# Kernel optimization log

Measured on AMD Instinct MI355X. Metric: run time of the kernel, lower is better.

The kernel has to match this reference:

```python
import jax, jax.numpy as jnp
import numpy as np

PS = 8; STRIDE = 4; KNN = 8; POOL_RATIO = 0.5; NHEADS = 4
EPS_BN = 1e-5; EPS_LN = 1e-5


def _conv(x, w, b):
    y = jax.lax.conv_general_dilated(x, w, (1, 1), ((1, 1), (1, 1)),
                                     dimension_numbers=('NCHW', 'OIHW', 'NCHW'))
    return y + b[None, :, None, None]


def _bn_eval(x, g, b):
    # BatchNorm2d in eval mode with running_mean=0, running_var=1
    return x * (g / np.sqrt(1.0 + EPS_BN))[None, :, None, None] + b[None, :, None, None]


def _maxpool2(x):
    return jax.lax.reduce_window(x, -jnp.inf, jax.lax.max, (1, 1, 2, 2), (1, 1, 2, 2), 'VALID')


def _layernorm(x, g, b):
    m = jnp.mean(x, axis=-1, keepdims=True)
    v = jnp.var(x, axis=-1, keepdims=True)
    return (x - m) / jnp.sqrt(v + EPS_LN) * g + b


def _mha(x, in_w, in_b, out_w, out_b):
    # batched self-attention, x: (B,S,E); matches nn.MultiheadAttention eval
    B, S, E = x.shape
    hd = E // NHEADS
    qkv = x @ in_w.T + in_b                      # (B,S,3E)
    q, k, v = jnp.split(qkv, 3, axis=-1)
    def heads(t):
        return t.reshape(B, S, NHEADS, hd).transpose(0, 2, 1, 3)
    q, k, v = heads(q), heads(k), heads(v)
    att = jax.nn.softmax(jnp.einsum('bhqd,bhkd->bhqk', q, k) / np.sqrt(hd), axis=-1)
    o = jnp.einsum('bhqk,bhkd->bhqd', att, v).transpose(0, 2, 1, 3).reshape(B, S, E)
    return o @ out_w.T + out_b


def _extract_patches(feat):
    # F.unfold(feat, kernel=PS, stride=STRIDE) -> (B, N, C*PS*PS), flat order (c, ki, kj)
    B, C, H, W = feat.shape
    nph = (H - PS) // STRIDE + 1
    npw = (W - PS) // STRIDE + 1
    hi = STRIDE * jnp.arange(nph)[:, None] + jnp.arange(PS)   # (nph, PS)
    wi = STRIDE * jnp.arange(npw)[:, None] + jnp.arange(PS)   # (npw, PS)
    p = feat[:, :, hi]            # (B,C,nph,PS,W)
    p = p[:, :, :, :, wi]         # (B,C,nph,PS,npw,PS)
    p = p.transpose(0, 2, 4, 1, 3, 5).reshape(B, nph * npw, C * PS * PS)
    return p, nph, npw


def _adjacency(nph, npw):
    # positions form a deterministic grid, identical across the batch -> static adjacency
    ii, jj = np.meshgrid(np.arange(nph), np.arange(npw), indexing='ij')
    pos = np.stack([ii.ravel(), jj.ravel()], axis=1).astype(np.float32)  # (N,2)
    N = pos.shape[0]
    d = np.linalg.norm(pos[:, None, :] - pos[None, :, :], axis=-1)
    order = np.argsort(d, axis=1, kind='stable')          # ascending; col 0 is self
    tgt = order[:, 1:KNN + 1]                             # (N, KNN)
    src = np.repeat(np.arange(N), KNN)
    adj = np.zeros((N, N), dtype=np.float32)
    adj[src, tgt.ravel()] = 1.0
    adj2 = ((adj @ adj) > 0).astype(np.float32)
    np.fill_diagonal(adj2, 0.0)
    return jnp.asarray(adj), jnp.asarray(adj2)


def setup_inputs() -> dict:
    key = jax.random.key(0)
    ks = jax.random.split(key, 16)
    def lin(k, o, i):
        return jax.random.normal(k, (o, i), jnp.float32) / np.sqrt(float(i))
    B = 16
    inp = {}
    inp['x'] = jax.random.normal(ks[0], (B, 3, 256, 256), jnp.float32)
    inp['conv1_w'] = jax.random.normal(ks[1], (64, 3, 3, 3), jnp.float32) / np.sqrt(27.0)
    inp['conv1_b'] = jnp.zeros((64,), jnp.float32)
    inp['bn1_g'] = jnp.ones((64,), jnp.float32); inp['bn1_b'] = jnp.zeros((64,), jnp.float32)
    inp['conv2_w'] = jax.random.normal(ks[2], (64, 64, 3, 3), jnp.float32) / np.sqrt(576.0)
    inp['conv2_b'] = jnp.zeros((64,), jnp.float32)
    inp['bn2_g'] = jnp.ones((64,), jnp.float32); inp['bn2_b'] = jnp.zeros((64,), jnp.float32)
    inp['proj_w'] = lin(ks[3], 128, 4096); inp['proj_b'] = jnp.zeros((128,), jnp.float32)
    inp['w1_w'] = lin(ks[4], 128, 128); inp['w1_b'] = jnp.zeros((128,), jnp.float32)
    inp['w2_w'] = lin(ks[5], 128, 128); inp['w2_b'] = jnp.zeros((128,), jnp.float32)
    inp['gate_w'] = lin(ks[6], 128, 256); inp['gate_b'] = jnp.zeros((128,), jnp.float32)
    inp['score_w'] = lin(ks[7], 1, 128); inp['score_b'] = jnp.zeros((1,), jnp.float32)
    inp['in_proj_w'] = lin(ks[8], 384, 128); inp['in_proj_b'] = jnp.zeros((384,), jnp.float32)
    inp['out_proj_w'] = lin(ks[9], 128, 128); inp['out_proj_b'] = jnp.zeros((128,), jnp.float32)
    inp['ff1_w'] = lin(ks[10], 512, 128); inp['ff1_b'] = jnp.zeros((512,), jnp.float32)
    inp['ff2_w'] = lin(ks[11], 128, 512); inp['ff2_b'] = jnp.zeros((128,), jnp.float32)
    inp['ln1_g'] = jnp.ones((128,), jnp.float32); inp['ln1_b'] = jnp.zeros((128,), jnp.float32)
    inp['ln2_g'] = jnp.ones((128,), jnp.float32); inp['ln2_b'] = jnp.zeros((128,), jnp.float32)
    inp['cls1_w'] = lin(ks[12], 64, 128); inp['cls1_b'] = jnp.zeros((64,), jnp.float32)
    inp['cls2_w'] = lin(ks[13], 2, 64); inp['cls2_b'] = jnp.zeros((2,), jnp.float32)
    return inp


def reference(x, conv1_w, conv1_b, bn1_g, bn1_b, conv2_w, conv2_b, bn2_g, bn2_b,
              proj_w, proj_b, w1_w, w1_b, w2_w, w2_b, gate_w, gate_b,
              score_w, score_b, in_proj_w, in_proj_b, out_proj_w, out_proj_b,
              ff1_w, ff1_b, ff2_w, ff2_b, ln1_g, ln1_b, ln2_g, ln2_b,
              cls1_w, cls1_b, cls2_w, cls2_b):
    # backbone
    feat = _maxpool2(jax.nn.relu(_bn_eval(_conv(x, conv1_w, conv1_b), bn1_g, bn1_b)))
    feat = _maxpool2(jax.nn.relu(_bn_eval(_conv(feat, conv2_w, conv2_b), bn2_g, bn2_b)))
    # patch graph construction (edges identical for every sample)
    patches, nph, npw = _extract_patches(feat)           # (B, N, 4096)
    adj1, adj2 = _adjacency(nph, npw)                    # (N, N) binary, static
    nodes = patches @ proj_w.T + proj_b                  # (B, N, 128)
    # multi-scale aggregation: index_add over edges == adj @ x (binary adjacency)
    z1 = jnp.einsum('ij,bjd->bid', adj1, nodes) @ w1_w.T + w1_b
    z2 = jnp.einsum('ij,bjd->bid', adj2, nodes) @ w2_w.T + w2_b
    g = jax.nn.sigmoid(jnp.concatenate([z1, z2], axis=-1) @ gate_w.T + gate_b)
    z = g * z1 + (1.0 - g) * z2                          # (B, N, 128)
    # hierarchical top-k pooling
    scores = (z @ score_w.T + score_b)[..., 0]           # (B, N)
    N = scores.shape[1]
    k = max(1, int(POOL_RATIO * N))
    _, idx = jax.lax.top_k(scores, k)                    # (B, k)
    pooled = jnp.take_along_axis(z, idx[..., None], axis=1)  # (B, k, 128)
    # graph transformer layer (dropout inactive in eval)
    h = _layernorm(pooled + _mha(pooled, in_proj_w, in_proj_b, out_proj_w, out_proj_b), ln1_g, ln1_b)
    ff = jax.nn.relu(h @ ff1_w.T + ff1_b) @ ff2_w.T + ff2_b
    h = _layernorm(h + ff, ln2_g, ln2_b)
    rep = jnp.sum(h, axis=1)                             # (B, 128)
    logits = jax.nn.relu(rep @ cls1_w.T + cls1_b) @ cls2_w.T + cls2_b
    return logits
```

## Files before the change

kernel.cpp:

```cpp
#include <hip/hip_runtime.h>
#include <hip/hip_bf16.h>
#include <math.h>

typedef unsigned short u16;
typedef unsigned int   u32;
typedef unsigned long long u64;
typedef __attribute__((ext_vector_type(8))) short short8v;
typedef __attribute__((ext_vector_type(4))) float f32x4;

__device__ __forceinline__ float bf2f(u16 u) {
  union { u32 i; float f; } v; v.i = ((u32)u) << 16; return v.f;
}
__device__ __forceinline__ u16 f2bf(float f) {
  union { float f; u32 i; } v; v.f = f;
  u32 r = (v.i + 0x7FFFu + ((v.i >> 16) & 1u)) >> 16;
  return (u16)r;
}

__global__ __launch_bounds__(256, 2) void k_conv1m(
    const float* __restrict__ x,
    const u16* __restrict__ wh, const u16* __restrict__ wl,
    const float* __restrict__ cb, const float* __restrict__ g, const float* __restrict__ bb,
    u16* __restrict__ feat1, int b0)
{
  __shared__ __align__(16) u16 sInH[3*18*18], sInL[3*18*18];
  __shared__ __align__(16) u16 sAh[256*40], sAl[256*40];
  __shared__ __align__(16) u16 sBh[64*40],  sBl[64*40];
  __shared__ float sBias[64];
  const int tx = blockIdx.x, ty = blockIdx.y, bl = blockIdx.z;
  const int b = b0 + bl;
  const int y0 = ty*16, x0 = tx*16;
  const int tid = threadIdx.x;
  const int w = tid >> 6, l = tid & 63, lr = l & 15, lk = l >> 4;

  if (tid < 64) {
    float sc = g[tid] * rsqrtf(1.0f + 1e-5f);
    sBias[tid] = cb[tid] * sc + bb[tid];
  }
  {
    const int oc = tid >> 2, seg = tid & 3;
    const int ps = seg ^ (oc & 3);
    *reinterpret_cast<uint4*>(&sBh[oc*40 + ps*8]) =
        *reinterpret_cast<const uint4*>(wh + oc*32 + seg*8);
    *reinterpret_cast<uint4*>(&sBl[oc*40 + ps*8]) =
        *reinterpret_cast<const uint4*>(wl + oc*32 + seg*8);
  }
  for (int i = tid; i < 3*18*18; i += 256) {
    const int c = i / 324, r = (i / 18) % 18, q = i % 18;
    const int yy = y0 - 1 + r, xx = x0 - 1 + q;
    float v = 0.f;
    if (yy >= 0 && yy < 256 && xx >= 0 && xx < 256)
      v = x[(((size_t)b*3 + c)*256 + yy)*256 + xx];
    const u16 h = f2bf(v);
    sInH[i] = h;
    sInL[i] = f2bf(v - bf2f(h));
  }
  __syncthreads();
  {
    const int py = tid >> 4, px = tid & 15;
    u32 hw[16], lw[16];
    #pragma unroll
    for (int i = 0; i < 16; i++) { hw[i] = 0u; lw[i] = 0u; }
    #pragma unroll
    for (int c = 0; c < 3; c++)
      #pragma unroll
      for (int ky = 0; ky < 3; ky++)
        #pragma unroll
        for (int kx = 0; kx < 3; kx++) {
          const int k = c*9 + ky*3 + kx;
          const int src = (c*18 + py + ky)*18 + px + kx;
          hw[k >> 1] |= ((u32)sInH[src]) << ((k & 1)*16);
          lw[k >> 1] |= ((u32)sInL[src]) << ((k & 1)*16);
        }
    #pragma unroll
    for (int s = 0; s < 4; s++) {
      const int ps = s ^ (tid & 3);
      uint4 vh, vl;
      vh.x = hw[s*4+0]; vh.y = hw[s*4+1]; vh.z = hw[s*4+2]; vh.w = hw[s*4+3];
      vl.x = lw[s*4+0]; vl.y = lw[s*4+1]; vl.z = lw[s*4+2]; vl.w = lw[s*4+3];
      *reinterpret_cast<uint4*>(&sAh[tid*40 + ps*8]) = vh;
      *reinterpret_cast<uint4*>(&sAl[tid*40 + ps*8]) = vl;
    }
  }
  __syncthreads();
  f32x4 acc[4][4];
  #pragma unroll
  for (int j = 0; j < 4; j++)
    #pragma unroll
    for (int ct = 0; ct < 4; ct++)
      acc[j][ct] = (f32x4){0.f,0.f,0.f,0.f};
  const int lkA = lk ^ (lr & 3);
  #pragma unroll
  for (int j = 0; j < 4; j++) {
    const int mt = w*4 + j;
    const short8v ah = *reinterpret_cast<const short8v*>(&sAh[(mt*16 + lr)*40 + lkA*8]);
    const short8v al = *reinterpret_cast<const short8v*>(&sAl[(mt*16 + lr)*40 + lkA*8]);
    #pragma unroll
    for (int ct = 0; ct < 4; ct++) {
      const short8v bh = *reinterpret_cast<const short8v*>(&sBh[(ct*16 + lr)*40 + lkA*8]);
      const short8v bv = *reinterpret_cast<const short8v*>(&sBl[(ct*16 + lr)*40 + lkA*8]);
      acc[j][ct] = __builtin_amdgcn_mfma_f32_16x16x32_bf16(ah, bh, acc[j][ct], 0, 0, 0);
      acc[j][ct] = __builtin_amdgcn_mfma_f32_16x16x32_bf16(ah, bv, acc[j][ct], 0, 0, 0);
      acc[j][ct] = __builtin_amdgcn_mfma_f32_16x16x32_bf16(al, bh, acc[j][ct], 0, 0, 0);
    }
  }
  #pragma unroll
  for (int j = 0; j < 2; j++) {
    const int jA = 2*j, jB = 2*j + 1;
    const int oy = ty*8 + w*2 + j;
    #pragma unroll
    for (int xh = 0; xh < 2; xh++) {
      const int ox = tx*8 + lk*2 + xh;
      #pragma unroll
      for (int ct = 0; ct < 4; ct++) {
        const int oc = ct*16 + lr;
        float m = fmaxf(fmaxf(acc[jA][ct][2*xh], acc[jA][ct][2*xh+1]),
                        fmaxf(acc[jB][ct][2*xh], acc[jB][ct][2*xh+1]));
        m = fmaxf(m + sBias[oc], 0.f);
        feat1[(((size_t)bl*128 + oy)*128 + ox)*64 + oc] = f2bf(m);
      }
    }
  }
}

__global__ __launch_bounds__(256, 2) void k_conv2m(
    const u16* __restrict__ feat1,
    const u16* __restrict__ wh, const u16* __restrict__ wl,
    const float* __restrict__ cb, const float* __restrict__ g, const float* __restrict__ bb,
    u16* __restrict__ feat2)
{
  __shared__ __align__(16) u16 sA[18*34*40];
  __shared__ __align__(16) u16 sBh[2][64*40], sBl[2][64*40];
  __shared__ float sBias[64];
  const int tx = blockIdx.x, ty = blockIdx.y, bl = blockIdx.z;
  const int y0 = ty*16, x0 = tx*32;
  const int tid = threadIdx.x;
  const int w = tid >> 6, l = tid & 63;
  const int lr = l & 15, lk = l >> 4;

  if (tid < 64) {
    float sc = g[tid] * rsqrtf(1.0f + 1e-5f);
    sBias[tid] = cb[tid] * sc + bb[tid];
  }

  f32x4 acc[8][4];
  #pragma unroll
  for (int j = 0; j < 8; j++)
    #pragma unroll
    for (int ct = 0; ct < 4; ct++)
      acc[j][ct] = (f32x4){0.f,0.f,0.f,0.f};

  const int ocB = tid >> 2;
  const int psB = (tid & 3) ^ (ocB & 3);
  uint4 rBh, rBl;
  auto ldB = [&](int chunk, int kk) {
    const size_t src = (size_t)(kk*2 + chunk)*2048 + tid*8;
    rBh = *reinterpret_cast<const uint4*>(wh + src);
    rBl = *reinterpret_cast<const uint4*>(wl + src);
  };
  auto stB = [&](int buf) {
    *reinterpret_cast<uint4*>(&sBh[buf][ocB*40 + psB*8]) = rBh;
    *reinterpret_cast<uint4*>(&sBl[buf][ocB*40 + psB*8]) = rBl;
  };

  const int lkB = lk ^ (lr & 3);
  for (int chunk = 0; chunk < 2; chunk++) {
    __syncthreads();
    ldB(chunk, 0);
    for (int idx = tid; idx < 612*4; idx += 256) {
      const int pix = idx >> 2, seg = idx & 3;
      const int r = pix / 34, cc = pix % 34;
      const int yy = y0 - 1 + r, xx = x0 - 1 + cc;
      uint4 v = {0u,0u,0u,0u};
      if (yy >= 0 && yy < 128 && xx >= 0 && xx < 128)
        v = *reinterpret_cast<const uint4*>(
              feat1 + (((size_t)bl*128 + yy)*128 + xx)*64 + chunk*32 + seg*8);
      const int ps = seg ^ (pix & 3);
      *reinterpret_cast<uint4*>(&sA[(size_t)pix*40 + ps*8]) = v;
    }
    stB(0);
    __syncthreads();
    int cur = 0;
    for (int kk = 0; kk < 9; kk++) {
      if (kk + 1 < 9) ldB(chunk, kk + 1);
      const int ky = kk / 3, kx = kk % 3;
      short8v a[8];
      #pragma unroll
      for (int j = 0; j < 8; j++) {
        const int m = w*8 + j;
        const int r = (m >> 1) + ky;
        const int cc = (m & 1)*16 + lr + kx;
        const int pixR = r*34 + cc;
        const int lkR = lk ^ (pixR & 3);
        a[j] = *reinterpret_cast<const short8v*>(&sA[(size_t)pixR*40 + lkR*8]);
      }
      #pragma unroll
      for (int ct = 0; ct < 4; ct++) {
        const short8v bh = *reinterpret_cast<const short8v*>(&sBh[cur][(ct*16 + lr)*40 + lkB*8]);
        const short8v bv = *reinterpret_cast<const short8v*>(&sBl[cur][(ct*16 + lr)*40 + lkB*8]);
        #pragma unroll
        for (int j = 0; j < 8; j++) {
          acc[j][ct] = __builtin_amdgcn_mfma_f32_16x16x32_bf16(a[j], bh, acc[j][ct], 0, 0, 0);
          acc[j][ct] = __builtin_amdgcn_mfma_f32_16x16x32_bf16(a[j], bv, acc[j][ct], 0, 0, 0);
        }
      }
      if (kk + 1 < 9) {
        stB(cur ^ 1);
        __syncthreads();
        cur ^= 1;
      }
    }
  }
  #pragma unroll
  for (int u = 0; u < 2; u++) {
    #pragma unroll
    for (int xh = 0; xh < 2; xh++) {
      const int jA = 4*u + xh, jB = 4*u + 2 + xh;
      #pragma unroll
      for (int ct = 0; ct < 4; ct++) {
        const int oc = ct*16 + lr;
        const float bias = sBias[oc];
        const float v0 = fmaxf(fmaxf(acc[jA][ct][0], acc[jA][ct][1]),
                               fmaxf(acc[jB][ct][0], acc[jB][ct][1]));
        const float v1 = fmaxf(fmaxf(acc[jA][ct][2], acc[jA][ct][3]),
                               fmaxf(acc[jB][ct][2], acc[jB][ct][3]));
        const u16 b0v = f2bf(fmaxf(v0 + bias, 0.f));
        const u16 b1v = f2bf(fmaxf(v1 + bias, 0.f));
        const int py = ty*8 + 2*w + u;
        const int px = tx*16 + xh*8 + lk*2;
        u32 pk = (u32)b0v | ((u32)b1v << 16);
        *reinterpret_cast<u32*>(&feat2[(((size_t)bl*64 + oc)*64 + py)*64 + px]) = pk;
      }
    }
  }
}

__global__ __launch_bounds__(256) void k_adj2(
    const int* __restrict__ nbr1, u64* __restrict__ mask2)
{
  const int i = threadIdx.x;
  if (i >= 225) return;
  u64 m0=0, m1=0, m2=0, m3=0;
  #pragma unroll
  for (int t = 0; t < 8; t++) {
    const int tt = nbr1[i*8 + t];
    #pragma unroll
    for (int u = 0; u < 8; u++) {
      const int j = nbr1[tt*8 + u];
      const u64 bset = 1ull << (j & 63);
      const int wd = j >> 6;
      m0 |= (wd == 0) ? bset : 0ull;
      m1 |= (wd == 1) ? bset : 0ull;
      m2 |= (wd == 2) ? bset : 0ull;
      m3 |= (wd == 3) ? bset : 0ull;
    }
  }
  {
    const u64 bc = ~(1ull << (i & 63));
    const int wd = i >> 6;
    if (wd == 0) m0 &= bc; else if (wd == 1) m1 &= bc;
    else if (wd == 2) m2 &= bc; else m3 &= bc;
  }
  mask2[i*4+0] = m0; mask2[i*4+1] = m1; mask2[i*4+2] = m2; mask2[i*4+3] = m3;
}

__global__ __launch_bounds__(256) void k_prep(
    const float* __restrict__ pjw, u16* __restrict__ pwh, u16* __restrict__ pwl,
    const float* __restrict__ c2w, const float* __restrict__ bn2g,
    u16* __restrict__ wc2h, u16* __restrict__ wc2l,
    const float* __restrict__ c1w, const float* __restrict__ bn1g,
    u16* __restrict__ wc1h, u16* __restrict__ wc1l,
    const float* __restrict__ ipw, float* __restrict__ iwt,
    const float* __restrict__ opw, float* __restrict__ owt,
    const float* __restrict__ f1w, float* __restrict__ f1wt,
    const float* __restrict__ f2w, float* __restrict__ f2wt,
    const float* __restrict__ w1w, float* __restrict__ w1t,
    const float* __restrict__ w2w, float* __restrict__ w2t,
    const float* __restrict__ gw,  float* __restrict__ gwt,
    int* __restrict__ nbr1)
{
  __shared__ int skey[256];
  __shared__ int sred[256];
  const int blk = blockIdx.x, tid = threadIdx.x;
  if (blk < 512) {
    const int i = (blk*256 + tid) * 4;
    float4 v = *reinterpret_cast<const float4*>(pjw + i);
    float e[4] = {v.x, v.y, v.z, v.w};
    ushort4 h, l;
    u16* hp = &h.x; u16* lp = &l.x;
    #pragma unroll
    for (int j = 0; j < 4; j++) {
      u16 hb = f2bf(e[j]);
      hp[j] = hb;
      lp[j] = f2bf(e[j] - bf2f(hb));
    }
    *reinterpret_cast<ushort4*>(pwh + i) = h;
    *reinterpret_cast<ushort4*>(pwl + i) = l;
  } else if (blk < 656) {
    const int d = (blk - 512)*256 + tid;
    if (d < 36864) {
      const int icL = d & 31, oc = (d >> 5) & 63, chunk = (d >> 11) & 1, kk = d >> 12;
      const float sc = bn2g[oc] * rsqrtf(1.0f + 1e-5f);
      const float val = c2w[((size_t)oc*64 + chunk*32 + icL)*9 + kk] * sc;
      const u16 hb = f2bf(val);
      wc2h[d] = hb;
      wc2l[d] = f2bf(val - bf2f(hb));
    }
  } else if (blk < 664) {
    const int d = (blk - 656)*256 + tid;
    if (d < 2048) {
      const int k = d & 31, oc = d >> 5;
      float val = 0.f;
      if (k < 27) val = c1w[oc*27 + k] * (bn1g[oc] * rsqrtf(1.0f + 1e-5f));
      const u16 hb = f2bf(val);
      wc1h[d] = hb;
      wc1l[d] = f2bf(val - bf2f(hb));
    }
  } else if (blk < 1688) {
    const float* src; float* dst; int O, K, base;
    if      (blk <  856) { src = ipw; dst = iwt;  O = 384; K = 128; base = 664;  }
    else if (blk <  920) { src = opw; dst = owt;  O = 128; K = 128; base = 856;  }
    else if (blk < 1176) { src = f1w; dst = f1wt; O = 512; K = 128; base = 920;  }
    else if (blk < 1432) { src = f2w; dst = f2wt; O = 128; K = 512; base = 1176; }
    else if (blk < 1496) { src = w1w; dst = w1t;  O = 128; K = 128; base = 1432; }
    else if (blk < 1560) { src = w2w; dst = w2t;  O = 128; K = 128; base = 1496; }
    else                 { src = gw;  dst = gwt;  O = 128; K = 256; base = 1560; }
    const int idx = (blk - base)*256 + tid;
    if (idx < O * K) {
      const int o = idx / K, k = idx % K;
      dst[(size_t)k * O + o] = src[idx];
    }
  } else {
    const int i = blk - 1688;
    int key = 0x7FFFFFFF;
    if (tid < 225 && tid != i) {
      const int di = i/15 - tid/15, dj = i%15 - tid%15;
      key = (di*di + dj*dj)*256 + tid;
    }
    skey[tid] = key;
    __syncthreads();
    for (int t = 0; t < 8; t++) {
      sred[tid] = skey[tid];
      __syncthreads();
      #pragma unroll
      for (int st = 128; st > 0; st >>= 1) {
        if (tid < st) sred[tid] = min(sred[tid], sred[tid+st]);
        __syncthreads();
      }
      const int wj = sred[0] & 255;
      if (tid == 0) nbr1[i*8 + t] = wj;
      __syncthreads();
      if (tid == wj) skey[tid] = 0x7FFFFFFF;
      __syncthreads();
    }
  }
}

__global__ __launch_bounds__(256, 2) void k_projm(
    const u16* __restrict__ feat2,
    const u16* __restrict__ pwh, const u16* __restrict__ pwl,
    float* __restrict__ partial, int b0)
{
  __shared__ __align__(16) u16 sBh[2][128*40];
  __shared__ __align__(16) u16 sBl[2][128*40];
  const int cx = blockIdx.x, kc = blockIdx.y, bl = blockIdx.z;
  const int b  = b0 + bl;
  const int n0 = cx * 64;
  const int rows = (225 - n0) < 64 ? (225 - n0) : 64;
  const int tid = threadIdx.x;
  const int w = tid >> 6, l = tid & 63;
  const int lr = l & 15, lk = l >> 4;

  f32x4 acc[8];
  #pragma unroll
  for (int i = 0; i < 8; i++) acc[i] = (f32x4){0.f, 0.f, 0.f, 0.f};

  int an = n0 + w*16 + lr;
  if (an > 224) an = 224;
  const int aph = an / 15, apw = an % 15;
  const int kbeg = kc * 512, kend = kbeg + 512;

  uint4 rBh[2], rBl[2];
  auto ldB = [&](int k0) {
    #pragma unroll
    for (int p = 0; p < 2; p++) {
      const int idx = p*256 + tid;
      const int col = idx >> 2, seg = idx & 3;
      const size_t off = (size_t)col*4096 + k0 + seg*8;
      rBh[p] = *reinterpret_cast<const uint4*>(pwh + off);
      rBl[p] = *reinterpret_cast<const uint4*>(pwl + off);
    }
  };
  auto stB = [&](int buf) {
    #pragma unroll
    for (int p = 0; p < 2; p++) {
      const int idx = p*256 + tid;
      const int col = idx >> 2, seg = idx & 3;
      const int ps = seg ^ (col & 3);
      *reinterpret_cast<uint4*>(&sBh[buf][col*40 + ps*8]) = rBh[p];
      *reinterpret_cast<uint4*>(&sBl[buf][col*40 + ps*8]) = rBl[p];
    }
  };

  const int lkB = lk ^ (lr & 3);
  ldB(kbeg);
  stB(0);
  __syncthreads();
  int cur = 0;
  for (int k0 = kbeg; k0 < kend; k0 += 32) {
    if (k0 + 32 < kend) ldB(k0 + 32);
    const int c = k0 >> 6;
    const int i = ((k0 & 32) >> 3) + lk;
    const u16* ap = feat2 + (((size_t)bl*64 + c)*64 + aph*4 + i)*64 + apw*4;
    union { short8v v; uint2 u[2]; } a;
    a.u[0] = *reinterpret_cast<const uint2*>(ap);
    a.u[1] = *reinterpret_cast<const uint2*>(ap + 4);
    #pragma unroll
    for (int ct = 0; ct < 8; ct++) {
      const short8v bh = *reinterpret_cast<const short8v*>(&sBh[cur][(ct*16 + lr)*40 + lkB*8]);
      const short8v bv = *reinterpret_cast<const short8v*>(&sBl[cur][(ct*16 + lr)*40 + lkB*8]);
      acc[ct] = __builtin_amdgcn_mfma_f32_16x16x32_bf16(a.v, bh, acc[ct], 0, 0, 0);
      acc[ct] = __builtin_amdgcn_mfma_f32_16x16x32_bf16(a.v, bv, acc[ct], 0, 0, 0);
    }
    if (k0 + 32 < kend) {
      stB(cur ^ 1);
      __syncthreads();
      cur ^= 1;
    }
  }
  #pragma unroll
  for (int ct = 0; ct < 8; ct++) {
    const int col = ct*16 + lr;
    #pragma unroll
    for (int v = 0; v < 4; v++) {
      const int r = w*16 + lk*4 + v;
      if (r < rows)
        partial[(((size_t)kc*16 + b)*225 + n0 + r)*128 + col] = acc[ct][v];
    }
  }
}

__global__ __launch_bounds__(128) void k_projr(
    const float* __restrict__ partial, const float* __restrict__ pb,
    float* __restrict__ nodes, int b0)
{
  const int n = blockIdx.x, bl = blockIdx.y;
  const int b = b0 + bl;
  const int d = threadIdx.x;
  float s = pb[d];
  #pragma unroll
  for (int kc = 0; kc < 8; kc++)
    s += partial[(((size_t)kc*16 + b)*225 + n)*128 + d];
  nodes[((size_t)b*225 + n)*128 + d] = s;
}

__global__ __launch_bounds__(256) void k_gz2(
    const float* __restrict__ nodes, const int* __restrict__ nbr1,
    const u64* __restrict__ mask2,
    const float* __restrict__ w1t, const float* __restrict__ w1b,
    const float* __restrict__ w2t, const float* __restrict__ w2b,
    const float* __restrict__ gwt, const float* __restrict__ gb,
    const float* __restrict__ sw, const float* __restrict__ sb,
    float* __restrict__ zbuf, float* __restrict__ scores)
{
  __shared__ float sA1[4][128], sA2[4][128], sC[4][256], sRed[4][128];
  const int row0 = blockIdx.x * 4;
  const int tid = threadIdx.x;
  const int d = tid & 127, rr = tid >> 7;
  #pragma unroll
  for (int q = 0; q < 2; q++) {
    const int lrow = rr*2 + q;
    const int row = row0 + lrow;
    const int b = row / 225, n = row % 225;
    const float* nb = nodes + (size_t)b * 225 * 128;
    float a1 = 0.f;
    #pragma unroll
    for (int t = 0; t < 8; t++) a1 += nb[(size_t)nbr1[n*8+t]*128 + d];
    float a2 = 0.f;
    for (int wd = 0; wd < 4; wd++) {
      u64 m = mask2[n*4 + wd];
      while (m) {
        int j = wd*64 + __builtin_ctzll(m);
        a2 += nb[(size_t)j*128 + d];
        m &= m - 1;
      }
    }
    sA1[lrow][d] = a1; sA2[lrow][d] = a2;
  }
  __syncthreads();
  float z1[2], z2[2];
  { const float b1 = w1b[d], b2 = w2b[d];
    z1[0] = b1; z1[1] = b1; z2[0] = b2; z2[1] = b2; }
  #pragma unroll 4
  for (int k = 0; k < 128; k++) {
    const float wv1 = w1t[k*128 + d];
    const float wv2 = w2t[k*128 + d];
    #pragma unroll
    for (int q = 0; q < 2; q++) {
      z1[q] += wv1 * sA1[rr*2 + q][k];
      z2[q] += wv2 * sA2[rr*2 + q][k];
    }
  }
  #pragma unroll
  for (int q = 0; q < 2; q++) {
    sC[rr*2 + q][d] = z1[q]; sC[rr*2 + q][128 + d] = z2[q];
  }
  __syncthreads();
  float gl[2];
  { const float bg = gb[d]; gl[0] = bg; gl[1] = bg; }
  #pragma unroll 4
  for (int k = 0; k < 256; k++) {
    const float wv = gwt[k*128 + d];
    #pragma unroll
    for (int q = 0; q < 2; q++)
      gl[q] += wv * sC[rr*2 + q][k];
  }
  const float swd = sw[d];
  #pragma unroll
  for (int q = 0; q < 2; q++) {
    const int row = row0 + rr*2 + q;
    const float gg = 1.f / (1.f + expf(-gl[q]));
    const float zv = gg * z1[q] + (1.f - gg) * z2[q];
    zbuf[(size_t)row*128 + d] = zv;
    sRed[rr*2 + q][d] = zv * swd;
  }
  __syncthreads();
  if (tid < 64) {
    const int r = tid >> 4, j = tid & 15;
    float part = 0.f;
    #pragma unroll
    for (int i = 0; i < 8; i++) part += sRed[r][j*8 + i];
    #pragma unroll
    for (int m = 8; m >= 1; m >>= 1) part += __shfl_xor(part, m, 64);
    if (j == 0) scores[row0 + r] = part + sb[0];
  }
}

__global__ __launch_bounds__(256) void k_topk(
    const float* __restrict__ scores, int* __restrict__ sel)
{
  __shared__ float ss[225];
  const int b = blockIdx.x, tid = threadIdx.x;
  if (tid < 112) sel[b*112 + tid] = tid;
  if (tid < 225) ss[tid] = scores[b*225 + tid];
  __syncthreads();
  if (tid < 225) {
    float s = ss[tid];
    int rank = 0;
    for (int j = 0; j < 225; j++) {
      float sj = ss[j];
      rank += (sj > s) || (sj == s && j < tid);
    }
    if (rank < 112) sel[b*112 + rank] = tid;
  }
}

__global__ __launch_bounds__(256) void k_qkv(
    const float* __restrict__ zbuf, const int* __restrict__ sel,
    const float* __restrict__ iwt, const float* __restrict__ ib,
    float* __restrict__ q, float* __restrict__ k, float* __restrict__ v)
{
  __shared__ float sx[7][128];
  const int s0 = blockIdx.x * 7, b = blockIdx.y;
  const int tid = threadIdx.x;
  const int c = tid & 127, half = tid >> 7;
  const int r0 = half * 4;
  const int nr = half ? 3 : 4;

  for (int idx = tid; idx < 7*128; idx += 256) {
    const int r = idx >> 7, dd = idx & 127;
    int row = sel[b*112 + s0 + r];
    row = row < 0 ? 0 : (row > 224 ? 224 : row);
    sx[r][dd] = zbuf[((size_t)b*225 + row)*128 + dd];
  }
  __syncthreads();

  float acc[3][4];
  #pragma unroll
  for (int p = 0; p < 3; p++)
    #pragma unroll
    for (int rr = 0; rr < 4; rr++) acc[p][rr] = ib[p*128 + c];
  for (int kk = 0; kk < 128; kk++) {
    float wv[3];
    #pragma unroll
    for (int p = 0; p < 3; p++) wv[p] = iwt[kk*384 + p*128 + c];
    #pragma unroll
    for (int rr = 0; rr < 4; rr++) {
      const int rowi = (r0 + rr < 7) ? (r0 + rr) : 6;
      const float xv = sx[rowi][kk];
      #pragma unroll
      for (int p = 0; p < 3; p++) acc[p][rr] += wv[p] * xv;
    }
  }
  const int h = c >> 5, t = c & 31;
  float* outs[3] = {q, k, v};
  #pragma unroll
  for (int p = 0; p < 3; p++)
    #pragma unroll
    for (int rr = 0; rr < 4; rr++)
      if (rr < nr)
        outs[p][(((size_t)b*4 + h)*112 + s0 + r0 + rr)*32 + t] = acc[p][rr];
}

__global__ __launch_bounds__(256) void k_attn(
    const float* __restrict__ q, const float* __restrict__ k,
    const float* __restrict__ v, float* __restrict__ o)
{
  __shared__ float sK[112*33], sV[112*33];
  __shared__ float sQ[14*33];
  __shared__ float sP[14][112];
  const int qc = blockIdx.x, h = blockIdx.y, b = blockIdx.z;
  const size_t base = ((size_t)b*4 + h) * 112 * 32;
  const int tid = threadIdx.x;
  for (int i = tid; i < 112*32; i += 256) {
    const int r = i >> 5, c = i & 31;
    sK[r*33 + c] = k[base + i];
    sV[r*33 + c] = v[base + i];
  }
  for (int i = tid; i < 14*32; i += 256) {
    const int r = i >> 5, c = i & 31;
    sQ[r*33 + c] = q[base + (size_t)(qc*14)*32 + i];
  }
  __syncthreads();
  const int qg = tid >> 4, j = tid & 15;
  if (qg < 14) {
    const float scale = 0.17677669529663687f;
    float pv[7];
    float mx = -INFINITY;
    #pragma unroll
    for (int t7 = 0; t7 < 7; t7++) {
      const int kk = j + t7*16;
      float s = 0.f;
      #pragma unroll
      for (int t = 0; t < 32; t++) s += sQ[qg*33 + t] * sK[kk*33 + t];
      pv[t7] = s * scale;
      mx = fmaxf(mx, pv[t7]);
    }
    #pragma unroll
    for (int m = 8; m >= 1; m >>= 1) mx = fmaxf(mx, __shfl_xor(mx, m, 16));
    float lsum = 0.f;
    #pragma unroll
    for (int t7 = 0; t7 < 7; t7++) { pv[t7] = expf(pv[t7] - mx); lsum += pv[t7]; }
    #pragma unroll
    for (int m = 8; m >= 1; m >>= 1) lsum += __shfl_xor(lsum, m, 16);
    const float inv = 1.f / lsum;
    #pragma unroll
    for (int t7 = 0; t7 < 7; t7++) sP[qg][j + t7*16] = pv[t7] * inv;
  }
  __syncthreads();
  if (qg < 14) {
    const int s = qc*14 + qg;
    float o0 = 0.f, o1 = 0.f;
    for (int kk = 0; kk < 112; kk++) {
      const float p = sP[qg][kk];
      o0 += p * sV[kk*33 + j];
      o1 += p * sV[kk*33 + j + 16];
    }
    float* op = o + ((size_t)b*112 + s)*128 + h*32;
    op[j] = o0;
    op[j + 16] = o1;
  }
}

__global__ __launch_bounds__(256) void k_tail(
    const float* __restrict__ o, const float* __restrict__ zbuf,
    const int* __restrict__ sel,
    const float* __restrict__ owt, const float* __restrict__ ob,
    const float* __restrict__ l1g, const float* __restrict__ l1b,
    const float* __restrict__ f1wt, const float* __restrict__ f1b,
    const float* __restrict__ f2wt, const float* __restrict__ f2b,
    const float* __restrict__ l2g, const float* __restrict__ l2b,
    float* __restrict__ h2)
{
  __shared__ float sO[7][128];
  __shared__ float sh[7][128];
  __shared__ float sf[7][512];
  __shared__ float sV[7][128];
  __shared__ float sMean[7], sRstd[7];
  const int s0 = blockIdx.x * 7, b = blockIdx.y;
  const int tid = threadIdx.x;
  const int d = tid & 127, half = tid >> 7;
  const int r0 = half * 4;
  const int nr = half ? 3 : 4;

  for (int idx = tid; idx < 7*128; idx += 256) {
    const int r = idx >> 7, dd = idx & 127;
    sO[r][dd] = o[((size_t)b*112 + s0 + r)*128 + dd];
  }
  __syncthreads();
  {
    float acc[4];
    #pragma unroll
    for (int rr = 0; rr < 4; rr++) acc[rr] = ob[d];
    for (int kk = 0; kk < 128; kk++) {
      const float wv = owt[kk*128 + d];
      #pragma unroll
      for (int rr = 0; rr < 4; rr++) {
        const int rowi = (r0 + rr < 7) ? (r0 + rr) : 6;
        acc[rr] += wv * sO[rowi][kk];
      }
    }
    #pragma unroll
    for (int rr = 0; rr < 4; rr++) {
      if (rr < nr) {
        int row = sel[b*112 + s0 + r0 + rr];
        row = row < 0 ? 0 : (row > 224 ? 224 : row);
        acc[rr] += zbuf[((size_t)b*225 + row)*128 + d];
        sV[r0 + rr][d] = acc[rr];
      }
    }
  }
  __syncthreads();
  {
    const int r = tid >> 4, j = tid & 15;
    if (r < 7) {
      float p1 = 0.f, p2 = 0.f;
      #pragma unroll
      for (int i = 0; i < 8; i++) { float v = sV[r][j*8 + i]; p1 += v; p2 += v*v; }
      #pragma unroll
      for (int m = 8; m >= 1; m >>= 1) {
        p1 += __shfl_xor(p1, m, 64);
        p2 += __shfl_xor(p2, m, 64);
      }
      if (j == 0) {
        const float mean = p1 * (1.f/128.f);
        sMean[r] = mean;
        sRstd[r] = rsqrtf(p2 * (1.f/128.f) - mean*mean + 1e-5f);
      }
    }
  }
  __syncthreads();
  for (int idx = tid; idx < 7*128; idx += 256) {
    const int r = idx >> 7, dd = idx & 127;
    sh[r][dd] = (sV[r][dd] - sMean[r]) * sRstd[r] * l1g[dd] + l1b[dd];
  }
  __syncthreads();

  {
    float a0[7], a1[7];
    const float b0 = f1b[tid], b1 = f1b[tid + 256];
    #pragma unroll
    for (int r = 0; r < 7; r++) { a0[r] = b0; a1[r] = b1; }
    for (int kk = 0; kk < 128; kk++) {
      const float w0 = f1wt[kk*512 + tid];
      const float w1 = f1wt[kk*512 + tid + 256];
      #pragma unroll
      for (int r = 0; r < 7; r++) {
        const float xv = sh[r][kk];
        a0[r] += w0 * xv;
        a1[r] += w1 * xv;
      }
    }
    #pragma unroll
    for (int r = 0; r < 7; r++) {
      sf[r][tid]       = fmaxf(a0[r], 0.f);
      sf[r][tid + 256] = fmaxf(a1[r], 0.f);
    }
  }
  __syncthreads();
  {
    float acc[4];
    #pragma unroll
    for (int rr = 0; rr < 4; rr++) acc[rr] = f2b[d];
    for (int kk = 0; kk < 512; kk++) {
      const float wv = f2wt[kk*128 + d];
      #pragma unroll
      for (int rr = 0; rr < 4; rr++) {
        const int rowi = (r0 + rr < 7) ? (r0 + rr) : 6;
        acc[rr] += wv * sf[rowi][kk];
      }
    }
    #pragma unroll
    for (int rr = 0; rr < 4; rr++)
      if (rr < nr)
        sV[r0 + rr][d] = sh[r0 + rr][d] + acc[rr];
  }
  __syncthreads();
  {
    const int r = tid >> 4, j = tid & 15;
    if (r < 7) {
      float p1 = 0.f, p2 = 0.f;
      #pragma unroll
      for (int i = 0; i < 8; i++) { float v = sV[r][j*8 + i]; p1 += v; p2 += v*v; }
      #pragma unroll
      for (int m = 8; m >= 1; m >>= 1) {
        p1 += __shfl_xor(p1, m, 64);
        p2 += __shfl_xor(p2, m, 64);
      }
      if (j == 0) {
        const float mean = p1 * (1.f/128.f);
        sMean[r] = mean;
        sRstd[r] = rsqrtf(p2 * (1.f/128.f) - mean*mean + 1e-5f);
      }
    }
  }
  __syncthreads();
  for (int idx = tid; idx < 7*128; idx += 256) {
    const int r = idx >> 7, dd = idx & 127;
    h2[((size_t)b*112 + s0 + r)*128 + dd] =
        (sV[r][dd] - sMean[r]) * sRstd[r] * l2g[dd] + l2b[dd];
  }
}

__global__ __launch_bounds__(64) void k_cls(
    const float* __restrict__ h2,
    const float* __restrict__ c1w, const float* __restrict__ c1b,
    const float* __restrict__ c2w, const float* __restrict__ c2b,
    float* __restrict__ out)
{
  __shared__ float sr[128], sc[64];
  const int b = blockIdx.x, tid = threadIdx.x;
  float r0 = 0.f, r1 = 0.f;
  for (int s2 = 0; s2 < 112; s2++) {
    const float* row = h2 + ((size_t)b*112 + s2)*128;
    r0 += row[tid];
    r1 += row[tid + 64];
  }
  sr[tid] = r0; sr[tid + 64] = r1;
  __syncthreads();
  float acc = c1b[tid];
  const float* wr = c1w + (size_t)tid * 128;
  for (int kk = 0; kk < 128; kk++) acc += wr[kk] * sr[kk];
  sc[tid] = fmaxf(acc, 0.f);
  __syncthreads();
  if (tid < 2) {
    float l = c2b[tid];
    for (int kk = 0; kk < 64; kk++) l += c2w[tid*64 + kk] * sc[kk];
    out[b*2 + tid] = l;
  }
}

extern "C" void kernel_launch(void* const* d_in, const int* in_sizes, int n_in,
                              void* d_out, int out_size, void* d_ws, size_t ws_size,
                              hipStream_t stream)
{
  const float* x    = (const float*)d_in[0];
  const float* c1w  = (const float*)d_in[1];
  const float* c1b  = (const float*)d_in[2];
  const float* bn1g = (const float*)d_in[3];
  const float* bn1b = (const float*)d_in[4];
  const float* c2w  = (const float*)d_in[5];
  const float* c2b  = (const float*)d_in[6];
  const float* bn2g = (const float*)d_in[7];
  const float* bn2b = (const float*)d_in[8];
  const float* pjw  = (const float*)d_in[9];
  const float* pjb  = (const float*)d_in[10];
  const float* w1w  = (const float*)d_in[11];
  const float* w1b  = (const float*)d_in[12];
  const float* w2w  = (const float*)d_in[13];
  const float* w2b  = (const float*)d_in[14];
  const float* gw   = (const float*)d_in[15];
  const float* gb   = (const float*)d_in[16];
  const float* scw  = (const float*)d_in[17];
  const float* scb  = (const float*)d_in[18];
  const float* ipw  = (const float*)d_in[19];
  const float* ipb  = (const float*)d_in[20];
  const float* opw  = (const float*)d_in[21];
  const float* opb  = (const float*)d_in[22];
  const float* f1w  = (const float*)d_in[23];
  const float* f1b  = (const float*)d_in[24];
  const float* f2w  = (const float*)d_in[25];
  const float* f2b  = (const float*)d_in[26];
  const float* l1g  = (const float*)d_in[27];
  const float* l1b  = (const float*)d_in[28];
  const float* l2g  = (const float*)d_in[29];
  const float* l2b  = (const float*)d_in[30];
  const float* cl1w = (const float*)d_in[31];
  const float* cl1b = (const float*)d_in[32];
  const float* cl2w = (const float*)d_in[33];
  const float* cl2b = (const float*)d_in[34];

  char* p = (char*)d_ws;
  auto alloc = [&](size_t n) { char* r = p; p += (n + 255) & ~(size_t)255; return r; };
  u64*   mask2  = (u64*)  alloc(900    * sizeof(u64));
  int*   nbr1   = (int*)  alloc(1800   * sizeof(int));
  int*   sel    = (int*)  alloc(1792   * sizeof(int));
  float* scores = (float*)alloc(3600   * sizeof(float));
  u16*   pwh    = (u16*)  alloc(524288 * sizeof(u16));
  u16*   pwl    = (u16*)  alloc(524288 * sizeof(u16));
  u16*   wc2h   = (u16*)  alloc(36864  * sizeof(u16));
  u16*   wc2l   = (u16*)  alloc(36864  * sizeof(u16));
  u16*   wc1h   = (u16*)  alloc(2048   * sizeof(u16));
  u16*   wc1l   = (u16*)  alloc(2048   * sizeof(u16));
  float* iwt    = (float*)alloc(49152  * sizeof(float));
  float* owt    = (float*)alloc(16384  * sizeof(float));
  float* f1wt   = (float*)alloc(65536  * sizeof(float));
  float* f2wt   = (float*)alloc(65536  * sizeof(float));
  float* w1t    = (float*)alloc(16384  * sizeof(float));
  float* w2t    = (float*)alloc(16384  * sizeof(float));
  float* gwt    = (float*)alloc(32768  * sizeof(float));
  float* partial= (float*)alloc(8ull*16*225*128 * sizeof(float));
  float* zbuf   = (float*)alloc(460800 * sizeof(float));
  float* nodes  = (float*)alloc(460800 * sizeof(float));
  const size_t fixed_bytes = (size_t)(p - (char*)d_ws);

  const size_t qkv_bytes = 3ull * 229376ull * sizeof(float);
  const size_t per_batch = 64ull*128*128*2 + 64ull*64*64*2;
  int BC = 16;
  size_t s3 = 0;
  for (;; BC >>= 1) {
    s3 = (size_t)BC * per_batch; if (s3 < qkv_bytes) s3 = qkv_bytes;
    if (fixed_bytes + s3 + 65536 <= ws_size) break;
    if (BC == 1) { return; }
  }
  char* S3 = alloc(s3);

  u16*   feat1 = (u16*)S3;
  u16*   feat2 = (u16*)(S3 + (size_t)BC * 2097152ull);
  float* qb    = (float*)S3;
  float* kb    = qb + 229376;
  float* vb    = kb + 229376;
  float* obuf  = nodes;
  float* hbuf  = nodes + 229376;

  k_prep<<<1913, 256, 0, stream>>>(pjw, pwh, pwl, c2w, bn2g, wc2h, wc2l,
                                   c1w, bn1g, wc1h, wc1l,
                                   ipw, iwt, opw, owt, f1w, f1wt, f2w, f2wt,
                                   w1w, w1t, w2w, w2t, gw, gwt, nbr1);
  k_adj2<<<1, 256, 0, stream>>>(nbr1, mask2);

  for (int b0 = 0; b0 < 16; b0 += BC) {
    k_conv1m<<<dim3(16,16,BC), 256, 0, stream>>>(x, wc1h, wc1l, c1b, bn1g, bn1b, feat1, b0);
    k_conv2m<<<dim3(4,8,BC), 256, 0, stream>>>(feat1, wc2h, wc2l, c2b, bn2g, bn2b, feat2);
    k_projm <<<dim3(4,8,BC), 256, 0, stream>>>(feat2, pwh, pwl, partial, b0);
    k_projr <<<dim3(225,BC), 128, 0, stream>>>(partial, pjb, nodes, b0);
  }

  k_gz2  <<<900, 256, 0, stream>>>(nodes, nbr1, mask2, w1t, w1b, w2t, w2b,
                                   gwt, gb, scw, scb, zbuf, scores);
  k_topk <<<16, 256, 0, stream>>>(scores, sel);
  k_qkv  <<<dim3(16,16), 256, 0, stream>>>(zbuf, sel, iwt, ipb, qb, kb, vb);
  k_attn <<<dim3(8,4,16), 256, 0, stream>>>(qb, kb, vb, obuf);
  k_tail <<<dim3(16,16), 256, 0, stream>>>(obuf, zbuf, sel, owt, opb, l1g, l1b,
                                           f1wt, f1b, f2wt, f2b, l2g, l2b, hbuf);
  k_cls  <<<16, 64, 0, stream>>>(hbuf, cl1w, cl1b, cl2w, cl2b, (float*)d_out);
}
```

Before: 260.6 us.

## Split projection GEMM tiles to 32 rows with 2x2 warp layout and prefetch A

The projection GEMM kernel now handles 32 node rows per block instead of 64, and its four waves are arranged as 2 row groups by 2 column groups, each owning 4 column tiles. The grid doubles along x, launch bounds allow 4 blocks per CU, and the A operand for the next k-step is loaded early alongside B. The goal is more blocks and higher occupancy for this small GEMM, plus hiding global A-load latency. In exchange, each B tile in shared memory is now loaded by twice as many blocks.

```diff
diff --git a/kernel.cpp b/kernel.cpp
--- a/kernel.cpp
+++ b/kernel.cpp
@@ -356,7 +356,7 @@
   }
 }
 
-__global__ __launch_bounds__(256, 2) void k_projm(
+__global__ __launch_bounds__(256, 4) void k_projm(
     const u16* __restrict__ feat2,
     const u16* __restrict__ pwh, const u16* __restrict__ pwl,
     float* __restrict__ partial, int b0)
@@ -365,17 +365,19 @@
   __shared__ __align__(16) u16 sBl[2][128*40];
   const int cx = blockIdx.x, kc = blockIdx.y, bl = blockIdx.z;
   const int b  = b0 + bl;
-  const int n0 = cx * 64;
-  const int rows = (225 - n0) < 64 ? (225 - n0) : 64;
+  const int n0 = cx * 32;
+  const int rows = (225 - n0) < 32 ? (225 - n0) : 32;
   const int tid = threadIdx.x;
   const int w = tid >> 6, l = tid & 63;
   const int lr = l & 15, lk = l >> 4;
-
-  f32x4 acc[8];
-  #pragma unroll
-  for (int i = 0; i < 8; i++) acc[i] = (f32x4){0.f, 0.f, 0.f, 0.f};
-
-  int an = n0 + w*16 + lr;
+  const int wr = w & 1;
+  const int wc = w >> 1;
+
+  f32x4 acc[4];
+  #pragma unroll
+  for (int i = 0; i < 4; i++) acc[i] = (f32x4){0.f, 0.f, 0.f, 0.f};
+
+  int an = n0 + wr*16 + lr;
   if (an > 224) an = 224;
   const int aph = an / 15, apw = an % 15;
   const int kbeg = kc * 512, kend = kbeg + 512;
@@ -401,41 +403,49 @@
       *reinterpret_cast<uint4*>(&sBl[buf][col*40 + ps*8]) = rBl[p];
     }
   };
-
-  const int lkB = lk ^ (lr & 3);
-  ldB(kbeg);
-  stB(0);
-  __syncthreads();
-  int cur = 0;
-  for (int k0 = kbeg; k0 < kend; k0 += 32) {
-    if (k0 + 32 < kend) ldB(k0 + 32);
+  auto ldA = [&](int k0, uint2& a0, uint2& a1) {
     const int c = k0 >> 6;
     const int i = ((k0 & 32) >> 3) + lk;
     const u16* ap = feat2 + (((size_t)bl*64 + c)*64 + aph*4 + i)*64 + apw*4;
+    a0 = *reinterpret_cast<const uint2*>(ap);
+    a1 = *reinterpret_cast<const uint2*>(ap + 4);
+  };
+
+  const int lkB = lk ^ (lr & 3);
+  uint2 a0c, a1c, a0n, a1n;
+  ldB(kbeg);
+  ldA(kbeg, a0c, a1c);
+  stB(0);
+  __syncthreads();
+  int cur = 0;
+  for (int k0 = kbeg; k0 < kend; k0 += 32) {
+    const bool more = (k0 + 32 < kend);
+    if (more) { ldB(k0 + 32); ldA(k0 + 32, a0n, a1n); }
     union { short8v v; uint2 u[2]; } a;
-    a.u[0] = *reinterpret_cast<const uint2*>(ap);
-    a.u[1] = *reinterpret_cast<const uint2*>(ap + 4);
-    #pragma unroll
-    for (int ct = 0; ct < 8; ct++) {
+    a.u[0] = a0c; a.u[1] = a1c;
+    #pragma unroll
+    for (int c4 = 0; c4 < 4; c4++) {
+      const int ct = wc*4 + c4;
       const short8v bh = *reinterpret_cast<const short8v*>(&sBh[cur][(ct*16 + lr)*40 + lkB*8]);
       const short8v bv = *reinterpret_cast<const short8v*>(&sBl[cur][(ct*16 + lr)*40 + lkB*8]);
-      acc[ct] = __builtin_amdgcn_mfma_f32_16x16x32_bf16(a.v, bh, acc[ct], 0, 0, 0);
-      acc[ct] = __builtin_amdgcn_mfma_f32_16x16x32_bf16(a.v, bv, acc[ct], 0, 0, 0);
-    }
-    if (k0 + 32 < kend) {
+      acc[c4] = __builtin_amdgcn_mfma_f32_16x16x32_bf16(a.v, bh, acc[c4], 0, 0, 0);
+      acc[c4] = __builtin_amdgcn_mfma_f32_16x16x32_bf16(a.v, bv, acc[c4], 0, 0, 0);
+    }
+    if (more) {
       stB(cur ^ 1);
       __syncthreads();
       cur ^= 1;
-    }
-  }
-  #pragma unroll
-  for (int ct = 0; ct < 8; ct++) {
-    const int col = ct*16 + lr;
+      a0c = a0n; a1c = a1n;
+    }
+  }
+  #pragma unroll
+  for (int c4 = 0; c4 < 4; c4++) {
+    const int col = (wc*4 + c4)*16 + lr;
     #pragma unroll
     for (int v = 0; v < 4; v++) {
-      const int r = w*16 + lk*4 + v;
+      const int r = wr*16 + lk*4 + v;
       if (r < rows)
-        partial[(((size_t)kc*16 + b)*225 + n0 + r)*128 + col] = acc[ct][v];
+        partial[(((size_t)kc*16 + b)*225 + n0 + r)*128 + col] = acc[c4][v];
     }
   }
 }
@@ -922,7 +932,7 @@
   for (int b0 = 0; b0 < 16; b0 += BC) {
     k_conv1m<<<dim3(16,16,BC), 256, 0, stream>>>(x, wc1h, wc1l, c1b, bn1g, bn1b, feat1, b0);
     k_conv2m<<<dim3(4,8,BC), 256, 0, stream>>>(feat1, wc2h, wc2l, c2b, bn2g, bn2b, feat2);
-    k_projm <<<dim3(4,8,BC), 256, 0, stream>>>(feat2, pwh, pwl, partial, b0);
+    k_projm <<<dim3(8,8,BC), 256, 0, stream>>>(feat2, pwh, pwl, partial, b0);
     k_projr <<<dim3(225,BC), 128, 0, stream>>>(partial, pjb, nodes, b0);
   }
 
```

After: 291.3 us. +11.8%, slower.
